# Optimization experiments

Hardware: AMD Instinct MI355X
Metric: run time of the kernel (lower is better)

## Reference

```python
import jax, jax.numpy as jnp
import numpy as np


def setup_inputs() -> dict:
    key = jax.random.key(0)
    k1, k2, k3 = jax.random.split(key, 3)
    B, S, D = 4, 2048, 1024
    x = jax.random.normal(k1, (B, S, D), dtype=jnp.float32)
    w_qkv = jax.random.normal(k2, (D, 3 * D), dtype=jnp.float32) * (D ** -0.5)
    b_qkv = jnp.zeros((3 * D,), dtype=jnp.float32)
    w_proj = jax.random.normal(k3, (D, D), dtype=jnp.float32) * (D ** -0.5)
    b_proj = jnp.zeros((D,), dtype=jnp.float32)
    return {"x": x, "w_qkv": w_qkv, "b_qkv": b_qkv, "w_proj": w_proj, "b_proj": b_proj}


def reference(x, w_qkv, b_qkv, w_proj, b_proj):
    B, S, D = x.shape
    H = 16
    hd = D // H
    scale = hd ** -0.5
    qkv = x @ w_qkv + b_qkv  # [B,S,3D]
    q, k, v = jnp.split(qkv, 3, axis=-1)
    # [B,S,D] -> [B,H,S,hd]
    q = q.reshape(B, S, H, hd).transpose(0, 2, 1, 3)
    k = k.reshape(B, S, H, hd).transpose(0, 2, 1, 3)
    v = v.reshape(B, S, H, hd).transpose(0, 2, 1, 3)
    attn = jnp.einsum('bhqd,bhkd->bhqk', q, k) * scale
    attn = jax.nn.softmax(attn, axis=-1)
    out = jnp.einsum('bhqk,bhkd->bhqd', attn, v)  # [B,H,S,hd]
    out = out.transpose(0, 2, 1, 3).reshape(B, S, D)
    return out @ w_proj + b_proj
```

## Files before the change

### kernel.cpp

```cpp
#include <hip/hip_runtime.h>
#include <stdint.h>

typedef __bf16 bf16x8 __attribute__((ext_vector_type(8)));
typedef float f32x4 __attribute__((ext_vector_type(4)));
typedef float f32x16 __attribute__((ext_vector_type(16)));
typedef unsigned short u16x8 __attribute__((ext_vector_type(8)));
typedef unsigned short u16x4 __attribute__((ext_vector_type(4)));

__device__ __forceinline__ unsigned short f2bf(float f) {
  union { float f; uint32_t u; } v; v.f = f;
  uint32_t r = v.u + 0x7FFFu + ((v.u >> 16) & 1u);
  return (unsigned short)(r >> 16);
}

__device__ __forceinline__ f32x4 mfma16(bf16x8 a, bf16x8 b, f32x4 c) {
  return __builtin_amdgcn_mfma_f32_16x16x32_bf16(a, b, c, 0, 0, 0);
}

__device__ __forceinline__ f32x16 mfma32(bf16x8 a, bf16x8 b, f32x16 c) {
  return __builtin_amdgcn_mfma_f32_32x32x16_bf16(a, b, c, 0, 0, 0);
}

__device__ __forceinline__ uint32_t cvtpk(float lo, float hi) {
  uint32_t r;
  asm("v_cvt_pk_bf16_f32 %0, %1, %2" : "=v"(r) : "v"(lo), "v"(hi));
  return r;
}

__device__ __forceinline__ void gload_lds16(const unsigned short* g, unsigned short* l) {
  __builtin_amdgcn_global_load_lds(
      (const __attribute__((address_space(1))) void*)g,
      (__attribute__((address_space(3))) void*)l, 16, 0, 0);
}

#define SCALEQ 0.18033688011112042f
#define FIXSHIFT 12.0f

__global__ __launch_bounds__(256) void preprocess(const float* __restrict__ x,
                                                  unsigned short* __restrict__ xbf,
                                                  const float* __restrict__ wqkv,
                                                  unsigned short* __restrict__ wTqkv,
                                                  const float* __restrict__ wproj,
                                                  unsigned short* __restrict__ wTproj) {
  __shared__ unsigned short tile[64][72];
  const int bid = blockIdx.x;
  const int t = threadIdx.x;
  if (bid < 4096) {
    int i = bid * 256 + t;
    const float4* p = (const float4*)x + (size_t)i * 2;
    float4 a = p[0], b = p[1];
    u16x8 o;
    o[0] = f2bf(a.x); o[1] = f2bf(a.y); o[2] = f2bf(a.z); o[3] = f2bf(a.w);
    o[4] = f2bf(b.x); o[5] = f2bf(b.y); o[6] = f2bf(b.z); o[7] = f2bf(b.w);
    *(u16x8*)&xbf[(size_t)i * 8] = o;
    return;
  }
  const float* w;
  unsigned short* wT;
  int K, N, n0, k0;
  if (bid < 4096 + 768) {
    int rb = bid - 4096;
    w = wqkv; wT = wTqkv; K = 1024; N = 3072;
    n0 = (rb % 48) * 64; k0 = (rb / 48) * 64;
  } else {
    int rb = bid - 4864;
    w = wproj; wT = wTproj; K = 1024; N = 1024;
    n0 = (rb % 16) * 64; k0 = (rb / 16) * 64;
  }
  {
    const int r = t >> 4, c0 = (t & 15) * 4;
#pragma unroll
    for (int i = 0; i < 4; ++i) {
      int rr = r + i * 16;
      float4 v = *(const float4*)&w[(size_t)(k0 + rr) * N + n0 + c0];
      tile[c0 + 0][rr] = f2bf(v.x);
      tile[c0 + 1][rr] = f2bf(v.y);
      tile[c0 + 2][rr] = f2bf(v.z);
      tile[c0 + 3][rr] = f2bf(v.w);
    }
  }
  __syncthreads();
  {
    const int c = t >> 2, r0 = (t & 3) * 16;
    u16x8 o1, o2;
#pragma unroll
    for (int i = 0; i < 8; ++i) { o1[i] = tile[c][r0 + i]; o2[i] = tile[c][r0 + 8 + i]; }
    *(u16x8*)&wT[(size_t)(n0 + c) * K + k0 + r0] = o1;
    *(u16x8*)&wT[(size_t)(n0 + c) * K + k0 + r0 + 8] = o2;
  }
}

__global__ __launch_bounds__(256) void qkv_gemm(const unsigned short* __restrict__ xbf,
                                                const unsigned short* __restrict__ wT,
                                                const float* __restrict__ bias,
                                                unsigned short* __restrict__ qb,
                                                unsigned short* __restrict__ kb,
                                                unsigned short* __restrict__ vf) {
  __shared__ unsigned short As[128 * 32];
  __shared__ unsigned short Bs[128 * 32];
  const int tid = threadIdx.x, lane = tid & 63, wave = tid >> 6;
  const int lin = blockIdx.y * 24 + blockIdx.x;
  const int swz = (lin & 7) * 192 + (lin >> 3);
  const int mb = (swz / 24) * 128, nb = (swz % 24) * 128;
  const int wr = (wave >> 1) * 64, wc = (wave & 1) * 64;
  const int fr = lane & 15, fk = (lane >> 4) * 8;
  f32x4 acc[4][4] = {};
  for (int kt = 0; kt < 1024; kt += 32) {
    __syncthreads();
#pragma unroll
    for (int i = 0; i < 2; ++i) {
      int ch = wave * 128 + i * 64 + lane;
      int r = ch >> 2, ko = (ch & 3) * 8;
      gload_lds16(xbf + (size_t)(mb + r) * 1024 + kt + ko, &As[(wave * 128 + i * 64) * 8]);
      gload_lds16(wT + (size_t)(nb + r) * 1024 + kt + ko, &Bs[(wave * 128 + i * 64) * 8]);
    }
    __syncthreads();
    bf16x8 a[4], bq[4];
#pragma unroll
    for (int m = 0; m < 4; ++m) a[m] = *(const bf16x8*)&As[(wr + m * 16 + fr) * 32 + fk];
#pragma unroll
    for (int n = 0; n < 4; ++n) bq[n] = *(const bf16x8*)&Bs[(wc + n * 16 + fr) * 32 + fk];
#pragma unroll
    for (int m = 0; m < 4; ++m)
#pragma unroll
      for (int n = 0; n < 4; ++n) acc[m][n] = mfma16(a[m], bq[n], acc[m][n]);
  }
#pragma unroll
  for (int m = 0; m < 4; ++m)
#pragma unroll
    for (int n = 0; n < 4; ++n) {
      int col = nb + wc + n * 16 + fr;
      float bv = bias[col];
      int type = col >> 10, cc = col & 1023, h = cc >> 6, d = cc & 63;
      int row0 = mb + wr + m * 16 + (lane >> 4) * 4;
      int bidx = row0 >> 11, s0 = row0 & 2047;
      int bh = bidx * 16 + h;
      if (type == 0) {
#pragma unroll
        for (int j4 = 0; j4 < 4; ++j4)
          qb[((size_t)bh * 2048 + s0 + j4) * 64 + d] = f2bf((acc[m][n][j4] + bv) * SCALEQ);
      } else if (type == 1) {
#pragma unroll
        for (int j4 = 0; j4 < 4; ++j4)
          kb[((size_t)bh * 2048 + s0 + j4) * 64 + d] = f2bf(acc[m][n][j4] + bv);
      } else {
        int t = s0 >> 5;
        int u = ((d >> 5) << 1) + ((s0 >> 4) & 1);
        int l = (((s0 >> 2) & 1) << 5) + (d & 31);
        int jj0 = ((s0 >> 3) & 1) << 2;
        u16x4 pk;
#pragma unroll
        for (int j4 = 0; j4 < 4; ++j4) pk[j4] = f2bf(acc[m][n][j4] + bv);
        *(u16x4*)&vf[((((size_t)bh * 64 + t) * 4 + u) * 64 + l) * 8 + jj0] = pk;
      }
    }
}

__global__ __launch_bounds__(256, 2) void attn_kernel(const unsigned short* __restrict__ qg,
                                                      const unsigned short* __restrict__ kgl,
                                                      const unsigned short* __restrict__ vf,
                                                      unsigned short* __restrict__ attnb) {
  const int tid = threadIdx.x;
  const int lane = tid & 63, wave = tid >> 6;
  const int l31 = lane & 31, hl = lane >> 5;
  const int h8 = hl * 8;

  const int L = blockIdx.y * 8 + blockIdx.x;
  const int xcd = L & 7, sl = L >> 3;
  const int bh = xcd * 8 + (sl & 7);
  const int qt = sl >> 3;
  const int b = bh >> 4, hh = bh & 15;

  const unsigned short* Qg = qg + (size_t)bh * 2048 * 64;
  const unsigned short* Kg = kgl + (size_t)bh * 2048 * 64;
  const unsigned short* VfB = vf + (size_t)bh * 131072 + lane * 8;
  const int q0 = qt * 256 + wave * 64;

  bf16x8 qf[2][4];
#pragma unroll
  for (int s2 = 0; s2 < 2; ++s2)
#pragma unroll
    for (int dw = 0; dw < 4; ++dw)
      qf[s2][dw] = *(const bf16x8*)&Qg[(size_t)(q0 + s2 * 32 + l31) * 64 + dw * 16 + h8];

  f32x16 o[2][2] = {};
  f32x4 lacc[2] = {};

  f32x16 cinit;
#pragma unroll
  for (int r = 0; r < 16; ++r) cinit[r] = -FIXSHIFT;

  union PU { uint32_t u[4]; bf16x8 v; };

  bf16x8 ka0, ka1, ka2, ka3, va0, va1, va2, va3;
  bf16x8 kb0, kb1, kb2, kb3, vb0, vb1, vb2, vb3;
  {
    const unsigned short* kr = &Kg[(size_t)l31 * 64 + h8];
    ka0 = *(const bf16x8*)&kr[0];
    ka1 = *(const bf16x8*)&kr[16];
    ka2 = *(const bf16x8*)&kr[32];
    ka3 = *(const bf16x8*)&kr[48];
    va0 = *(const bf16x8*)&VfB[0];
    va1 = *(const bf16x8*)&VfB[512];
    va2 = *(const bf16x8*)&VfB[1024];
    va3 = *(const bf16x8*)&VfB[1536];
  }

#define STEP(K0, K1, K2, K3, V0, V1, V2, V3)                                  \
  {                                                                           \
    _Pragma("unroll")                                                         \
    for (int s2 = 0; s2 < 2; ++s2) {                                          \
      f32x16 sa = mfma32(K0, qf[s2][0], cinit);                               \
      sa = mfma32(K1, qf[s2][1], sa);                                         \
      sa = mfma32(K2, qf[s2][2], sa);                                         \
      sa = mfma32(K3, qf[s2][3], sa);                                         \
      _Pragma("unroll")                                                       \
      for (int r = 0; r < 16; ++r) sa[r] = __builtin_amdgcn_exp2f(sa[r]);     \
      _Pragma("unroll")                                                       \
      for (int j = 0; j < 4; ++j)                                             \
        lacc[s2][j] += (sa[j] + sa[4 + j]) + (sa[8 + j] + sa[12 + j]);        \
      PU p0, p1;                                                              \
      p0.u[0] = cvtpk(sa[0], sa[1]);   p0.u[1] = cvtpk(sa[2], sa[3]);         \
      p0.u[2] = cvtpk(sa[4], sa[5]);   p0.u[3] = cvtpk(sa[6], sa[7]);         \
      p1.u[0] = cvtpk(sa[8], sa[9]);   p1.u[1] = cvtpk(sa[10], sa[11]);       \
      p1.u[2] = cvtpk(sa[12], sa[13]); p1.u[3] = cvtpk(sa[14], sa[15]);       \
      o[s2][0] = mfma32(V0, p0.v, o[s2][0]);                                  \
      o[s2][0] = mfma32(V1, p1.v, o[s2][0]);                                  \
      o[s2][1] = mfma32(V2, p0.v, o[s2][1]);                                  \
      o[s2][1] = mfma32(V3, p1.v, o[s2][1]);                                  \
    }                                                                         \
  }

  for (int t = 0; t < 64; t += 2) {
    {
      const unsigned short* kr = &Kg[(size_t)((t + 1) * 32 + l31) * 64 + h8];
      const unsigned short* vp = VfB + (size_t)(t + 1) * 2048;
      kb0 = *(const bf16x8*)&kr[0];
      kb1 = *(const bf16x8*)&kr[16];
      kb2 = *(const bf16x8*)&kr[32];
      kb3 = *(const bf16x8*)&kr[48];
      vb0 = *(const bf16x8*)&vp[0];
      vb1 = *(const bf16x8*)&vp[512];
      vb2 = *(const bf16x8*)&vp[1024];
      vb3 = *(const bf16x8*)&vp[1536];
    }
    STEP(ka0, ka1, ka2, ka3, va0, va1, va2, va3);
    if (t + 2 < 64) {
      const unsigned short* kr = &Kg[(size_t)((t + 2) * 32 + l31) * 64 + h8];
      const unsigned short* vp = VfB + (size_t)(t + 2) * 2048;
      ka0 = *(const bf16x8*)&kr[0];
      ka1 = *(const bf16x8*)&kr[16];
      ka2 = *(const bf16x8*)&kr[32];
      ka3 = *(const bf16x8*)&kr[48];
      va0 = *(const bf16x8*)&vp[0];
      va1 = *(const bf16x8*)&vp[512];
      va2 = *(const bf16x8*)&vp[1024];
      va3 = *(const bf16x8*)&vp[1536];
    }
    STEP(kb0, kb1, kb2, kb3, vb0, vb1, vb2, vb3);
  }
#undef STEP

#pragma unroll
  for (int s2 = 0; s2 < 2; ++s2) {
    float l = (lacc[s2][0] + lacc[s2][1]) + (lacc[s2][2] + lacc[s2][3]);
    l += __shfl_xor(l, 32);
    float invl = 1.0f / l;
    const size_t base = ((size_t)(b * 2048 + q0 + s2 * 32 + l31)) * 1024 + hh * 64;
#pragma unroll
    for (int g = 0; g < 4; ++g) {
      u16x4 w0, w1;
#pragma unroll
      for (int j = 0; j < 4; ++j) {
        w0[j] = f2bf(o[s2][0][g * 4 + j] * invl);
        w1[j] = f2bf(o[s2][1][g * 4 + j] * invl);
      }
      int d = 8 * g + 4 * hl;
      *(u16x4*)&attnb[base + d] = w0;
      *(u16x4*)&attnb[base + 32 + d] = w1;
    }
  }
}

__global__ __launch_bounds__(256) void proj_gemm(const unsigned short* __restrict__ abf,
                                                 const unsigned short* __restrict__ wT,
                                                 const float* __restrict__ bias,
                                                 float* __restrict__ outp) {
  __shared__ unsigned short As[128 * 32];
  __shared__ unsigned short Bs[128 * 32];
  const int tid = threadIdx.x, lane = tid & 63, wave = tid >> 6;
  const int lin = blockIdx.y * 8 + blockIdx.x;
  const int swz = (lin & 7) * 64 + (lin >> 3);
  const int mb = (swz >> 3) * 128, nb = (swz & 7) * 128;
  const int wr = (wave >> 1) * 64, wc = (wave & 1) * 64;
  const int fr = lane & 15, fk = (lane >> 4) * 8;
  f32x4 acc[4][4] = {};
  for (int kt = 0; kt < 1024; kt += 32) {
    __syncthreads();
#pragma unroll
    for (int i = 0; i < 2; ++i) {
      int ch = wave * 128 + i * 64 + lane;
      int r = ch >> 2, ko = (ch & 3) * 8;
      gload_lds16(abf + (size_t)(mb + r) * 1024 + kt + ko, &As[(wave * 128 + i * 64) * 8]);
      gload_lds16(wT + (size_t)(nb + r) * 1024 + kt + ko, &Bs[(wave * 128 + i * 64) * 8]);
    }
    __syncthreads();
    bf16x8 a[4], bq[4];
#pragma unroll
    for (int m = 0; m < 4; ++m) a[m] = *(const bf16x8*)&As[(wr + m * 16 + fr) * 32 + fk];
#pragma unroll
    for (int n = 0; n < 4; ++n) bq[n] = *(const bf16x8*)&Bs[(wc + n * 16 + fr) * 32 + fk];
#pragma unroll
    for (int m = 0; m < 4; ++m)
#pragma unroll
      for (int n = 0; n < 4; ++n) acc[m][n] = mfma16(a[m], bq[n], acc[m][n]);
  }
#pragma unroll
  for (int m = 0; m < 4; ++m)
#pragma unroll
    for (int n = 0; n < 4; ++n) {
      int col = nb + wc + n * 16 + fr;
      float bv = bias[col];
#pragma unroll
      for (int j = 0; j < 4; ++j) {
        int row = mb + wr + m * 16 + (lane >> 4) * 4 + j;
        outp[(size_t)row * 1024 + col] = acc[m][n][j] + bv;
      }
    }
}

extern "C" void kernel_launch(void* const* d_in, const int* in_sizes, int n_in,
                              void* d_out, int out_size, void* d_ws, size_t ws_size,
                              hipStream_t stream) {
  const float* x = (const float*)d_in[0];
  const float* w_qkv = (const float*)d_in[1];
  const float* b_qkv = (const float*)d_in[2];
  const float* w_proj = (const float*)d_in[3];
  const float* b_proj = (const float*)d_in[4];
  float* outp = (float*)d_out;
  char* ws = (char*)d_ws;

  const size_t OFF_XBF = 0;
  const size_t OFF_WTQKV = 16777216;
  const size_t OFF_WTPROJ = 23068672;
  const size_t OFF_Q = 25165824;
  const size_t OFF_K = 41943040;
  const size_t OFF_VF = 58720256;
  const size_t NEED = 75497472;
  if (ws_size < NEED) return;

  unsigned short* xbf = (unsigned short*)(ws + OFF_XBF);
  unsigned short* wTqkv = (unsigned short*)(ws + OFF_WTQKV);
  unsigned short* wTproj = (unsigned short*)(ws + OFF_WTPROJ);
  unsigned short* qbuf = (unsigned short*)(ws + OFF_Q);
  unsigned short* kbuf = (unsigned short*)(ws + OFF_K);
  unsigned short* vfbuf = (unsigned short*)(ws + OFF_VF);
  unsigned short* attnb = xbf;

  hipLaunchKernelGGL(preprocess, dim3(5120), dim3(256), 0, stream,
                     x, xbf, w_qkv, wTqkv, w_proj, wTproj);
  hipLaunchKernelGGL(qkv_gemm, dim3(24, 64), dim3(256), 0, stream, xbf, wTqkv, b_qkv, qbuf, kbuf, vfbuf);
  hipLaunchKernelGGL(attn_kernel, dim3(8, 64), dim3(256), 0, stream, qbuf, kbuf, vfbuf, attnb);
  hipLaunchKernelGGL(proj_gemm, dim3(8, 64), dim3(256), 0, stream, attnb, wTproj, b_proj, outp);
}
```

Measured before the change: 201.2 us.

## Halve per-wave query rows in attention and double grid for occupancy

Each wave in the attention kernel now handles 32 query rows instead of 64, so each block covers 128 queries and the grid doubles to 1024 blocks. Launch bounds rise to 4 blocks per CU, cutting the register footprint to raise occupancy and improve latency hiding. In exchange, every K/V fragment loaded from global memory is reused for only one query tile instead of two, which doubles K/V load traffic per unit of work.

```diff
diff --git a/kernel.cpp b/kernel.cpp
--- a/kernel.cpp
+++ b/kernel.cpp
@@ -156,7 +156,7 @@
     }
 }
 
-__global__ __launch_bounds__(256, 2) void attn_kernel(const unsigned short* __restrict__ qg,
+__global__ __launch_bounds__(256, 4) void attn_kernel(const unsigned short* __restrict__ qg,
                                                       const unsigned short* __restrict__ kgl,
                                                       const unsigned short* __restrict__ vf,
                                                       unsigned short* __restrict__ attnb) {
@@ -165,7 +165,7 @@
   const int l31 = lane & 31, hl = lane >> 5;
   const int h8 = hl * 8;
 
-  const int L = blockIdx.y * 8 + blockIdx.x;
+  const int L = blockIdx.y * 16 + blockIdx.x;
   const int xcd = L & 7, sl = L >> 3;
   const int bh = xcd * 8 + (sl & 7);
   const int qt = sl >> 3;
@@ -174,17 +174,15 @@
   const unsigned short* Qg = qg + (size_t)bh * 2048 * 64;
   const unsigned short* Kg = kgl + (size_t)bh * 2048 * 64;
   const unsigned short* VfB = vf + (size_t)bh * 131072 + lane * 8;
-  const int q0 = qt * 256 + wave * 64;
-
-  bf16x8 qf[2][4];
-#pragma unroll
-  for (int s2 = 0; s2 < 2; ++s2)
-#pragma unroll
-    for (int dw = 0; dw < 4; ++dw)
-      qf[s2][dw] = *(const bf16x8*)&Qg[(size_t)(q0 + s2 * 32 + l31) * 64 + dw * 16 + h8];
-
-  f32x16 o[2][2] = {};
-  f32x4 lacc[2] = {};
+  const int q0 = qt * 128 + wave * 32;
+
+  bf16x8 qf[4];
+#pragma unroll
+  for (int dw = 0; dw < 4; ++dw)
+    qf[dw] = *(const bf16x8*)&Qg[(size_t)(q0 + l31) * 64 + dw * 16 + h8];
+
+  f32x16 o0 = {}, o1 = {};
+  f32x4 lacc = {};
 
   f32x16 cinit;
 #pragma unroll
@@ -208,27 +206,24 @@
 
 #define STEP(K0, K1, K2, K3, V0, V1, V2, V3)                                  \
   {                                                                           \
+    f32x16 sa = mfma32(K0, qf[0], cinit);                                     \
+    sa = mfma32(K1, qf[1], sa);                                               \
+    sa = mfma32(K2, qf[2], sa);                                               \
+    sa = mfma32(K3, qf[3], sa);                                               \
     _Pragma("unroll")                                                         \
-    for (int s2 = 0; s2 < 2; ++s2) {                                          \
-      f32x16 sa = mfma32(K0, qf[s2][0], cinit);                               \
-      sa = mfma32(K1, qf[s2][1], sa);                                         \
-      sa = mfma32(K2, qf[s2][2], sa);                                         \
-      sa = mfma32(K3, qf[s2][3], sa);                                         \
-      _Pragma("unroll")                                                       \
-      for (int r = 0; r < 16; ++r) sa[r] = __builtin_amdgcn_exp2f(sa[r]);     \
-      _Pragma("unroll")                                                       \
-      for (int j = 0; j < 4; ++j)                                             \
-        lacc[s2][j] += (sa[j] + sa[4 + j]) + (sa[8 + j] + sa[12 + j]);        \
-      PU p0, p1;                                                              \
-      p0.u[0] = cvtpk(sa[0], sa[1]);   p0.u[1] = cvtpk(sa[2], sa[3]);         \
-      p0.u[2] = cvtpk(sa[4], sa[5]);   p0.u[3] = cvtpk(sa[6], sa[7]);         \
-      p1.u[0] = cvtpk(sa[8], sa[9]);   p1.u[1] = cvtpk(sa[10], sa[11]);       \
-      p1.u[2] = cvtpk(sa[12], sa[13]); p1.u[3] = cvtpk(sa[14], sa[15]);       \
-      o[s2][0] = mfma32(V0, p0.v, o[s2][0]);                                  \
-      o[s2][0] = mfma32(V1, p1.v, o[s2][0]);                                  \
-      o[s2][1] = mfma32(V2, p0.v, o[s2][1]);                                  \
-      o[s2][1] = mfma32(V3, p1.v, o[s2][1]);                                  \
-    }                                                                         \
+    for (int r = 0; r < 16; ++r) sa[r] = __builtin_amdgcn_exp2f(sa[r]);       \
+    _Pragma("unroll")                                                         \
+    for (int j = 0; j < 4; ++j)                                               \
+      lacc[j] += (sa[j] + sa[4 + j]) + (sa[8 + j] + sa[12 + j]);              \
+    PU p0, p1;                                                                \
+    p0.u[0] = cvtpk(sa[0], sa[1]);   p0.u[1] = cvtpk(sa[2], sa[3]);           \
+    p0.u[2] = cvtpk(sa[4], sa[5]);   p0.u[3] = cvtpk(sa[6], sa[7]);           \
+    p1.u[0] = cvtpk(sa[8], sa[9]);   p1.u[1] = cvtpk(sa[10], sa[11]);         \
+    p1.u[2] = cvtpk(sa[12], sa[13]); p1.u[3] = cvtpk(sa[14], sa[15]);         \
+    o0 = mfma32(V0, p0.v, o0);                                                \
+    o0 = mfma32(V1, p1.v, o0);                                                \
+    o1 = mfma32(V2, p0.v, o1);                                                \
+    o1 = mfma32(V3, p1.v, o1);                                                \
   }
 
   for (int t = 0; t < 64; t += 2) {
@@ -261,19 +256,18 @@
   }
 #undef STEP
 
-#pragma unroll
-  for (int s2 = 0; s2 < 2; ++s2) {
-    float l = (lacc[s2][0] + lacc[s2][1]) + (lacc[s2][2] + lacc[s2][3]);
+  {
+    float l = (lacc[0] + lacc[1]) + (lacc[2] + lacc[3]);
     l += __shfl_xor(l, 32);
     float invl = 1.0f / l;
-    const size_t base = ((size_t)(b * 2048 + q0 + s2 * 32 + l31)) * 1024 + hh * 64;
+    const size_t base = ((size_t)(b * 2048 + q0 + l31)) * 1024 + hh * 64;
 #pragma unroll
     for (int g = 0; g < 4; ++g) {
       u16x4 w0, w1;
 #pragma unroll
       for (int j = 0; j < 4; ++j) {
-        w0[j] = f2bf(o[s2][0][g * 4 + j] * invl);
-        w1[j] = f2bf(o[s2][1][g * 4 + j] * invl);
+        w0[j] = f2bf(o0[g * 4 + j] * invl);
+        w1[j] = f2bf(o1[g * 4 + j] * invl);
       }
       int d = 8 * g + 4 * hl;
       *(u16x4*)&attnb[base + d] = w0;
@@ -360,6 +354,6 @@
   hipLaunchKernelGGL(preprocess, dim3(5120), dim3(256), 0, stream,
                      x, xbf, w_qkv, wTqkv, w_proj, wTproj);
   hipLaunchKernelGGL(qkv_gemm, dim3(24, 64), dim3(256), 0, stream, xbf, wTqkv, b_qkv, qbuf, kbuf, vfbuf);
-  hipLaunchKernelGGL(attn_kernel, dim3(8, 64), dim3(256), 0, stream, qbuf, kbuf, vfbuf, attnb);
+  hipLaunchKernelGGL(attn_kernel, dim3(16, 64), dim3(256), 0, stream, qbuf, kbuf, vfbuf, attnb);
   hipLaunchKernelGGL(proj_gemm, dim3(8, 64), dim3(256), 0, stream, attnb, wTproj, b_proj, outp);
 }
```

New measurement: 322.4 us. +60.2%, slower.
